# Kernel optimization log

Measured on AMD Instinct MI355X. Metric: run time of the kernel, lower is better.

The kernel has to match this reference:

```python
import math
import jax, jax.numpy as jnp
import numpy as np

DIM = 2048
SLOTS = 256
T = 64          # num_replay_steps
N = 8192        # number of episodic traces
REPLAY_NOISE = 0.01
FREQ = 6.0      # theta frequency (Hz)
DT = 0.01
STRENGTH = 0.5  # write strength used in consolidate()
THRESHOLD = 0.0


def setup_inputs() -> dict:
    key = jax.random.key(0)
    ks = jax.random.split(key, 16)
    def w(k, shape):
        return (jax.random.normal(k, shape, jnp.float32) / math.sqrt(shape[-1]))
    return {
        "traces": jax.random.normal(ks[0], (N, DIM), jnp.float32),
        "noise": jax.random.normal(ks[1], (T, DIM), jnp.float32),
        "memory0": jax.random.normal(ks[2], (SLOTS, DIM), jnp.float32) * 0.01,
        "usage0": jnp.zeros((SLOTS,), jnp.float32),
        "W1": w(ks[3], (DIM, DIM)), "b1": jnp.zeros((DIM,), jnp.float32),
        "W2": w(ks[4], (DIM, DIM)), "b2": jnp.zeros((DIM,), jnp.float32),
        "Wl": w(ks[5], (DIM, DIM)), "bl": jnp.zeros((DIM,), jnp.float32),
        "vw": jax.random.normal(ks[6], (DIM,), jnp.float32),
        "vb": jnp.zeros((DIM,), jnp.float32),
        "Wg": w(ks[7], (DIM, DIM)), "bg": jnp.zeros((DIM,), jnp.float32),
        "Wa": w(ks[8], (SLOTS, DIM)), "ba": jnp.zeros((SLOTS,), jnp.float32),
        "We": w(ks[9], (DIM, DIM)), "be": jnp.zeros((DIM,), jnp.float32),
        "Wad": w(ks[10], (DIM, DIM)), "bad": jnp.zeros((DIM,), jnp.float32),
        "idx": jax.random.randint(ks[11], (T,), 0, N, jnp.int64 if jax.config.jax_enable_x64 else jnp.int32),
    }


def reference(traces, noise, memory0, usage0, W1, b1, W2, b2, Wl, bl, vw, vb,
              Wg, bg, Wa, ba, We, be, Wad, bad, idx):
    # Deterministic theta phase schedule (step_theta per replay step).
    t = jnp.arange(T, dtype=jnp.float32)
    phase = jnp.mod(2.0 * math.pi * FREQ * DT * (t + 1.0), 2.0 * math.pi)  # (T,)

    # --- batched (parallel) part: replay transform + NMDA gate + heads ---
    trace = traces[idx]                                   # (T, DIM) gather
    noisy = trace + noise * REPLAY_NOISE
    h = jax.nn.relu(noisy @ W1.T + b1)
    x = h @ W2.T + b2                                     # transformed (T, DIM)

    ligand = jax.nn.sigmoid(x @ Wl.T + bl)                # (T, DIM)
    phase_signal = jnp.cos(phase - math.pi)[:, None]      # (T, 1)
    voltage = jax.nn.sigmoid(phase_signal * vw[None, :] + vb - THRESHOLD)
    gate = jax.nn.sigmoid((ligand * voltage) @ Wg.T + bg)
    gated = x * gate                                      # (T, DIM)

    logits0 = gated @ Wa.T + ba                           # (T, SLOTS)
    erase = jax.nn.sigmoid(gated @ We.T + be)             # (T, DIM)
    add = gated @ Wad.T + bad                             # (T, DIM)

    # --- sequential part: erase/add outer-product writes with usage penalty ---
    def step(carry, inputs):
        mem, usage = carry
        lg, er, ad = inputs
        wgt = jax.nn.softmax(lg - usage * 0.1)            # (SLOTS,)
        outer_w = STRENGTH * wgt[:, None]                 # (SLOTS, 1)
        mem = mem * (1.0 - outer_w * er[None, :]) + outer_w * ad[None, :]
        return (mem, usage + wgt), None

    (mem, usage), _ = jax.lax.scan(step, (memory0, usage0), (logits0, erase, add))
    return mem
```

## Files before the change

kernel.cpp:

```cpp
#include <hip/hip_runtime.h>
#include <math.h>

#define DIM 2048
#define SLOTS 256
#define TSTEPS 64
#define FB (TSTEPS * DIM)
#define KQ 8
#define KS (DIM / KQ)
#define BK 64
#define NC (KS / BK)
#define JG 32

typedef unsigned short u16;
typedef __bf16 bf16x8 __attribute__((ext_vector_type(8)));
typedef float f32x4 __attribute__((ext_vector_type(4)));

union FragU { unsigned u[4]; bf16x8 v; };

__device__ __forceinline__ u16 f2bf(float f){
    union { float f; unsigned u; } v; v.f = f;
    unsigned r = v.u + 0x7fffu + ((v.u >> 16) & 1u);
    return (u16)(r >> 16);
}
__device__ __forceinline__ float sigmoidf_(float x){ return 1.0f / (1.0f + __expf(-x)); }

__device__ __forceinline__ void split8t(const float* x, bf16x8& hi, bf16x8& lo){
    FragU H, L;
    #pragma unroll
    for (int p = 0; p < 4; ++p){
        union { float f; unsigned u; } u0, u1, l0, l1;
        u0.f = x[2*p]; u1.f = x[2*p+1];
        unsigned h0 = u0.u & 0xffff0000u, h1 = u1.u & 0xffff0000u;
        H.u[p] = (h0 >> 16) | h1;
        l0.f = u0.f - __uint_as_float(h0);
        l1.f = u1.f - __uint_as_float(h1);
        L.u[p] = (l0.u >> 16) | (l1.u & 0xffff0000u);
    }
    hi = H.v; lo = L.v;
}

__device__ __forceinline__ f32x4 mfma16(bf16x8 a, bf16x8 b, f32x4 c){
    return __builtin_amdgcn_mfma_f32_16x16x32_bf16(a, b, c, 0, 0, 0);
}

__device__ __forceinline__ void gl_lds16(const float* gp, float* lp){
    __builtin_amdgcn_global_load_lds(
        (const __attribute__((address_space(1))) unsigned int*)gp,
        (__attribute__((address_space(3))) unsigned int*)lp, 16, 0, 0);
}

__device__ __forceinline__ void calib_inline(int lane, int w, int* trr, int* jrr){
    const u16 oneb = 0x3F80;
    const u16 lb = f2bf((float)((lane & 15) + 1));
    FragU O, L;
    #pragma unroll
    for (int p = 0; p < 4; ++p){
        O.u[p] = ((unsigned)oneb) | (((unsigned)oneb) << 16);
        L.u[p] = ((unsigned)lb)   | (((unsigned)lb)   << 16);
    }
    f32x4 z = {0.f, 0.f, 0.f, 0.f};
    f32x4 dj = mfma16(O.v, L.v, z);
    f32x4 dt = mfma16(L.v, O.v, z);
    #pragma unroll
    for (int r = 0; r < 4; ++r){
        int jl = (int)(dj[r] * (1.0f/32.0f) + 0.5f) - 1;
        int tl = (int)(dt[r] * (1.0f/32.0f) + 0.5f) - 1;
        trr[r] = w * 16 + (tl & 15);
        jrr[r] = jl & 15;
    }
}

struct GSm { float A[NC * 64 * BK]; float Wb[2][16 * BK]; };

__device__ __forceinline__ void gemm_block(const float* __restrict__ A,
                                           const float* __restrict__ Wg0,
                                           int kq, GSm& sm, f32x4* acc)
{
    const int tid = threadIdx.x;
    const int lane = tid & 63, w = tid >> 6;
    const int s = lane & 15, rsub = lane >> 4;
    const int n4 = lane & 15;
    const int kbase = kq * KS;

    #pragma unroll
    for (int c = 0; c < NC; ++c)
        #pragma unroll
        for (int i = 0; i < 4; ++i){
            const int rowL = w * 16 + i * 4 + rsub;
            const float* gp = A + (size_t)rowL * DIM + kbase + c * BK + ((s ^ (rowL & 15)) << 2);
            gl_lds16(gp, sm.A + (c * 64 + w * 16 + i * 4) * BK);
        }
    {
        const int rowL = w * 4 + rsub;
        const float* gp = Wg0 + (size_t)rowL * DIM + kbase + ((s ^ (rowL & 15)) << 2);
        gl_lds16(gp, sm.Wb[0] + (w * 4) * BK);
    }
    __syncthreads();

    acc[0] = (f32x4){0.f, 0.f, 0.f, 0.f};
    acc[1] = (f32x4){0.f, 0.f, 0.f, 0.f};

    #pragma unroll
    for (int it = 0; it < 2 * NC; ++it){
        const int jt = it >> 2, c = it & 3;
        const int bufc = it & 1;
        if (it + 1 < 2 * NC){
            const int nj = (it + 1) >> 2, ncc = (it + 1) & 3;
            const int rowL = w * 4 + rsub;
            const float* gp = Wg0 + (size_t)(nj * 16 + rowL) * DIM
                            + kbase + ncc * BK + ((s ^ (rowL & 15)) << 2);
            gl_lds16(gp, sm.Wb[bufc ^ 1] + (w * 4) * BK);
        }
        const float* At = sm.A + c * 64 * BK;
        const float* Wt = sm.Wb[bufc];
        #pragma unroll
        for (int ks = 0; ks < 2; ++ks){
            const int cg0 = ks * 8 + (lane >> 4) * 2;
            const int rA = w * 16 + n4;
            float a8[8], w8[8];
            *(float4*)(a8)     = *(const float4*)&At[rA * BK + ((cg0 ^ n4) << 2)];
            *(float4*)(a8 + 4) = *(const float4*)&At[rA * BK + (((cg0 + 1) ^ n4) << 2)];
            *(float4*)(w8)     = *(const float4*)&Wt[n4 * BK + ((cg0 ^ n4) << 2)];
            *(float4*)(w8 + 4) = *(const float4*)&Wt[n4 * BK + (((cg0 + 1) ^ n4) << 2)];
            bf16x8 ah, al, wh, wl;
            split8t(a8, ah, al);
            split8t(w8, wh, wl);
            if (jt == 0){
                acc[0] = mfma16(ah, wh, acc[0]);
                acc[0] = mfma16(al, wh, acc[0]);
                acc[0] = mfma16(ah, wl, acc[0]);
            } else {
                acc[1] = mfma16(ah, wh, acc[1]);
                acc[1] = mfma16(al, wh, acc[1]);
                acc[1] = mfma16(ah, wl, acc[1]);
            }
        }
        __syncthreads();
    }
}

__global__ __launch_bounds__(256)
void gemm_s(const float* __restrict__ A, const float* __restrict__ W,
            float* __restrict__ Pp)
{
    __shared__ GSm sm;
    const int kq = blockIdx.x & (KQ - 1);
    const int jg = blockIdx.x >> 3;
    const int j0 = jg * JG;
    const int lane = threadIdx.x & 63, w = threadIdx.x >> 6;
    int trr[4], jrr[4];
    calib_inline(lane, w, trr, jrr);
    f32x4 acc[2];
    gemm_block(A, W + (size_t)j0 * DIM, kq, sm, acc);
    float* outb = Pp + (size_t)kq * FB;
    #pragma unroll
    for (int jt = 0; jt < 2; ++jt)
        #pragma unroll
        for (int r = 0; r < 4; ++r)
            outb[(size_t)trr[r] * DIM + j0 + jt * 16 + jrr[r]] = acc[jt][r];
}

__global__ __launch_bounds__(256)
void gemm_h(const float* __restrict__ G,
            const float* __restrict__ We, const float* __restrict__ Wad,
            const float* __restrict__ Wa,
            float* __restrict__ PpE, float* __restrict__ PpA, float* __restrict__ PpL)
{
    __shared__ GSm sm;
    const int kq = blockIdx.x & (KQ - 1);
    const int jg = blockIdx.x >> 3;
    const float* W; float* out; int j0, NJ;
    if (jg < 64)       { W = We;  out = PpE; j0 = jg * JG;        NJ = DIM; }
    else if (jg < 128) { W = Wad; out = PpA; j0 = (jg - 64) * JG; NJ = DIM; }
    else               { W = Wa;  out = PpL; j0 = (jg - 128) * JG; NJ = SLOTS; }
    const int lane = threadIdx.x & 63, w = threadIdx.x >> 6;
    int trr[4], jrr[4];
    calib_inline(lane, w, trr, jrr);
    f32x4 acc[2];
    gemm_block(G, W + (size_t)j0 * DIM, kq, sm, acc);
    float* outb = out + (size_t)kq * 64 * NJ;
    #pragma unroll
    for (int jt = 0; jt < 2; ++jt)
        #pragma unroll
        for (int r = 0; r < 4; ++r)
            outb[(size_t)trr[r] * NJ + j0 + jt * 16 + jrr[r]] = acc[jt][r];
}

template<int MODE>
__device__ __forceinline__ void comb_core(int bb, const float* __restrict__ P,
    const float* __restrict__ bias, const float* __restrict__ vwp,
    const float* __restrict__ vbp, const float* __restrict__ Xp,
    float* __restrict__ out)
{
    const size_t i0 = ((size_t)bb * 256 + threadIdx.x) * 8;
    const int t = (int)(i0 >> 11);
    const int j = (int)(i0 & (DIM - 1));
    float v[8], tmp[8];
    *(float4*)(v)     = *(const float4*)(P + i0);
    *(float4*)(v + 4) = *(const float4*)(P + i0 + 4);
    #pragma unroll
    for (int p = 1; p < KQ; ++p){
        *(float4*)(tmp)     = *(const float4*)(P + (size_t)p * FB + i0);
        *(float4*)(tmp + 4) = *(const float4*)(P + (size_t)p * FB + i0 + 4);
        #pragma unroll
        for (int c = 0; c < 8; ++c) v[c] += tmp[c];
    }
    float b8[8];
    *(float4*)(b8)     = *(const float4*)(bias + j);
    *(float4*)(b8 + 4) = *(const float4*)(bias + j + 4);
    float x8[8], y8[8];
    if (MODE == 2){
        *(float4*)(x8)     = *(const float4*)(vwp + j);
        *(float4*)(x8 + 4) = *(const float4*)(vwp + j + 4);
        *(float4*)(y8)     = *(const float4*)(vbp + j);
        *(float4*)(y8 + 4) = *(const float4*)(vbp + j + 4);
    }
    if (MODE == 3){
        *(float4*)(x8)     = *(const float4*)(Xp + i0);
        *(float4*)(x8 + 4) = *(const float4*)(Xp + i0 + 4);
    }
    const float ps = -cosf(0.37699111843077515f * (float)(t + 1));
    float r[8];
    #pragma unroll
    for (int c = 0; c < 8; ++c){
        float u = v[c] + b8[c];
        if (MODE == 0)      r[c] = fmaxf(u, 0.f);
        else if (MODE == 1) r[c] = u;
        else if (MODE == 2) r[c] = sigmoidf_(u) * sigmoidf_(fmaf(ps, x8[c], y8[c]));
        else if (MODE == 3) r[c] = x8[c] * sigmoidf_(u);
        else                r[c] = sigmoidf_(u);
    }
    *(float4*)(out + i0)     = *(const float4*)(r);
    *(float4*)(out + i0 + 4) = *(const float4*)(r + 4);
}

template<int MODE>
__global__ __launch_bounds__(256)
void comb8(const float* __restrict__ P, const float* __restrict__ bias,
           const float* __restrict__ vwp, const float* __restrict__ vbp,
           const float* __restrict__ Xp, float* __restrict__ out)
{
    comb_core<MODE>((int)blockIdx.x, P, bias, vwp, vbp, Xp, out);
}

__global__ __launch_bounds__(256)
void comb_ea_scan(const float* __restrict__ PpE, const float* __restrict__ be,
                  const float* __restrict__ PpA, const float* __restrict__ bad_,
                  const float* __restrict__ PpL, const float* __restrict__ ba,
                  const float* __restrict__ usage0,
                  float* __restrict__ ER, float* __restrict__ AD,
                  float* __restrict__ WG)
{
    const int b = (int)blockIdx.x;
    if (b < 64){
        comb_core<4>(b, PpE, be, nullptr, nullptr, nullptr, ER);
        return;
    }
    if (b < 128){
        comb_core<1>(b - 64, PpA, bad_, nullptr, nullptr, nullptr, AD);
        return;
    }
    const int tid = threadIdx.x;
    if (tid >= 64) return;
    const int PS = TSTEPS * SLOTS;
    float u[4], bv[4], cur[4];
    #pragma unroll
    for (int c = 0; c < 4; ++c){
        const int sl = tid + 64 * c;
        u[c]  = usage0[sl];
        bv[c] = ba[sl];
        float s = bv[c];
        #pragma unroll
        for (int p = 0; p < KQ; ++p) s += PpL[p * PS + sl];
        cur[c] = s;
    }
    for (int t = 0; t < TSTEPS; ++t){
        float nxt[4] = {0.f, 0.f, 0.f, 0.f};
        if (t < TSTEPS - 1){
            #pragma unroll
            for (int c = 0; c < 4; ++c){
                const int sl = (t + 1) * SLOTS + tid + 64 * c;
                float s = bv[c];
                #pragma unroll
                for (int p = 0; p < KQ; ++p) s += PpL[p * PS + sl];
                nxt[c] = s;
            }
        }
        float e[4];
        #pragma unroll
        for (int c = 0; c < 4; ++c) e[c] = __expf(cur[c] - 0.1f * u[c]);
        float sm_ = (e[0] + e[1]) + (e[2] + e[3]);
        #pragma unroll
        for (int off = 1; off < 64; off <<= 1) sm_ += __shfl_xor(sm_, off, 64);
        float inv = 1.0f / sm_;
        float* wr = WG + t * SLOTS;
        #pragma unroll
        for (int c = 0; c < 4; ++c){
            float ww = e[c] * inv;
            u[c] += ww;
            wr[tid + 64 * c] = ww;
        }
        #pragma unroll
        for (int c = 0; c < 4; ++c) cur[c] = nxt[c];
    }
}

__global__ __launch_bounds__(256)
void init_k(const float* __restrict__ traces, const float* __restrict__ noise,
            const int* __restrict__ idxw, float* __restrict__ A0)
{
    const int tid = threadIdx.x;
    __shared__ int i64f;
    int v = 0;
    if (tid < 32) v = (idxw[2 * tid + 1] != 0) ? 1 : 0;
    unsigned long long bm = __ballot(v);
    if (tid == 0) i64f = (bm == 0ull) ? 1 : 0;
    __syncthreads();
    const int t = blockIdx.x;
    long row = i64f ? (long)idxw[2 * t] : (long)idxw[t];
    const int k = tid * 8;
    const float* tr = traces + (size_t)row * DIM + k;
    const float* nz = noise + (size_t)t * DIM + k;
    float4 a0 = *(const float4*)(tr), a1 = *(const float4*)(tr + 4);
    float4 b0 = *(const float4*)(nz), b1 = *(const float4*)(nz + 4);
    float4 r0, r1;
    r0.x = fmaf(0.01f, b0.x, a0.x); r0.y = fmaf(0.01f, b0.y, a0.y);
    r0.z = fmaf(0.01f, b0.z, a0.z); r0.w = fmaf(0.01f, b0.w, a0.w);
    r1.x = fmaf(0.01f, b1.x, a1.x); r1.y = fmaf(0.01f, b1.y, a1.y);
    r1.z = fmaf(0.01f, b1.z, a1.z); r1.w = fmaf(0.01f, b1.w, a1.w);
    float* o = A0 + (size_t)t * DIM + k;
    *(float4*)(o) = r0; *(float4*)(o + 4) = r1;
}

__global__ __launch_bounds__(256)
void mem_k(const float* __restrict__ mem0, const float* __restrict__ wgt,
           const float* __restrict__ ER, const float* __restrict__ AD,
           float* __restrict__ out)
{
    const int s = threadIdx.x;
    const int d0 = blockIdx.x * 8;
    float m[8];
    *(float4*)(m)     = *(const float4*)(mem0 + (size_t)s * DIM + d0);
    *(float4*)(m + 4) = *(const float4*)(mem0 + (size_t)s * DIM + d0 + 4);
    for (int t = 0; t < TSTEPS; ++t){
        const size_t ro = (size_t)t * DIM + d0;
        float e8[8], a8[8];
        *(float4*)(e8)     = *(const float4*)(ER + ro);
        *(float4*)(e8 + 4) = *(const float4*)(ER + ro + 4);
        *(float4*)(a8)     = *(const float4*)(AD + ro);
        *(float4*)(a8 + 4) = *(const float4*)(AD + ro + 4);
        float w = 0.5f * wgt[t * SLOTS + s];
        #pragma unroll
        for (int c = 0; c < 8; ++c){
            float f = w * e8[c];
            float tmp = fmaf(-f, m[c], m[c]);
            m[c] = fmaf(w, a8[c], tmp);
        }
    }
    float* op = out + (size_t)s * DIM + d0;
    *(float4*)(op)     = *(const float4*)(m);
    *(float4*)(op + 4) = *(const float4*)(m + 4);
}

extern "C" void kernel_launch(void* const* d_in, const int* in_sizes, int n_in,
                              void* d_out, int out_size, void* d_ws, size_t ws_size,
                              hipStream_t stream)
{
    const float* traces = (const float*)d_in[0];
    const float* noise  = (const float*)d_in[1];
    const float* mem0   = (const float*)d_in[2];
    const float* usage0 = (const float*)d_in[3];
    const float* W1 = (const float*)d_in[4];  const float* b1 = (const float*)d_in[5];
    const float* W2 = (const float*)d_in[6];  const float* b2 = (const float*)d_in[7];
    const float* Wl = (const float*)d_in[8];  const float* bl = (const float*)d_in[9];
    const float* vw = (const float*)d_in[10]; const float* vb = (const float*)d_in[11];
    const float* Wg = (const float*)d_in[12]; const float* bg = (const float*)d_in[13];
    const float* Wa = (const float*)d_in[14]; const float* ba = (const float*)d_in[15];
    const float* We = (const float*)d_in[16]; const float* be = (const float*)d_in[17];
    const float* Wad = (const float*)d_in[18]; const float* bad_ = (const float*)d_in[19];
    const int* idx = (const int*)d_in[20];

    float* pool = (float*)d_ws;
    float* A0v = pool + 0 * (size_t)FB;
    float* Hv  = pool + 1 * (size_t)FB;
    float* Xv  = pool + 2 * (size_t)FB;
    float* LVv = pool + 3 * (size_t)FB;
    float* Gv  = pool + 4 * (size_t)FB;
    float* ERv = pool + 5 * (size_t)FB;
    float* ADv = pool + 6 * (size_t)FB;
    float* Pp  = pool + 7 * (size_t)FB;
    float* PpE = pool + 15 * (size_t)FB;
    float* PpA = pool + 23 * (size_t)FB;
    float* PpL = pool + 31 * (size_t)FB;
    float* WGv = pool + 32 * (size_t)FB;

    init_k<<<TSTEPS, 256, 0, stream>>>(traces, noise, idx, A0v);

    gemm_s<<<64 * KQ, 256, 0, stream>>>(A0v, W1, Pp);
    comb8<0><<<64, 256, 0, stream>>>(Pp, b1, nullptr, nullptr, nullptr, Hv);
    gemm_s<<<64 * KQ, 256, 0, stream>>>(Hv, W2, Pp);
    comb8<1><<<64, 256, 0, stream>>>(Pp, b2, nullptr, nullptr, nullptr, Xv);
    gemm_s<<<64 * KQ, 256, 0, stream>>>(Xv, Wl, Pp);
    comb8<2><<<64, 256, 0, stream>>>(Pp, bl, vw, vb, nullptr, LVv);
    gemm_s<<<64 * KQ, 256, 0, stream>>>(LVv, Wg, Pp);
    comb8<3><<<64, 256, 0, stream>>>(Pp, bg, nullptr, nullptr, Xv, Gv);

    gemm_h<<<136 * KQ, 256, 0, stream>>>(Gv, We, Wad, Wa, PpE, PpA, PpL);
    comb_ea_scan<<<129, 256, 0, stream>>>(PpE, be, PpA, bad_, PpL, ba, usage0,
                                          ERv, ADv, WGv);
    mem_k<<<DIM / 8, 256, 0, stream>>>(mem0, WGv, ERv, ADv, (float*)d_out);
}
```

Baseline: 290.1 us.

## Fuse gather into first GEMM and fuse scan, combine and memory update

The gather-plus-noise step is folded into the first GEMM's A-tile load, so the init kernel and its round trip through global memory go away. The softmax scan, the erase/add split-K reduction and the memory update are merged into one kernel. Each of its 256 blocks recomputes the softmax weights into shared memory and reduces the partial sums on the fly. W-tile staging switches from async global-to-LDS loads to register prefetch two chunks ahead, with explicit barriers. The cost is redundant scan work in every block and more global reads of the partial sums per block, in exchange for two fewer launches and fewer intermediate buffers.

Measured after the change: 416.8 us. 1.44x slower.

```diff
diff --git a/kernel.cpp b/kernel.cpp
--- a/kernel.cpp
+++ b/kernel.cpp
@@ -72,9 +72,18 @@
 
 struct GSm { float A[NC * 64 * BK]; float Wb[2][16 * BK]; };
 
-__device__ __forceinline__ void gemm_block(const float* __restrict__ A,
-                                           const float* __restrict__ Wg0,
-                                           int kq, GSm& sm, f32x4* acc)
+__device__ __forceinline__ const float* waddr(const float* Wg0, int kbase, int chunk,
+                                              int w, int rsub, int s){
+    const int rowL = w * 4 + rsub;
+    const int nj = chunk >> 2, ncc = chunk & 3;
+    return Wg0 + (size_t)(nj * 16 + rowL) * DIM + kbase + ncc * BK + ((s ^ rowL) << 2);
+}
+
+template<int GATHER>
+__device__ __forceinline__ void gemm_core(const float* __restrict__ A,
+    const float* __restrict__ traces, const float* __restrict__ noise,
+    const int* __restrict__ idxw, int i64f,
+    const float* __restrict__ Wg0, int kq, GSm& sm, f32x4* acc)
 {
     const int tid = threadIdx.x;
     const int lane = tid & 63, w = tid >> 6;
@@ -82,19 +91,35 @@
     const int n4 = lane & 15;
     const int kbase = kq * KS;
 
-    #pragma unroll
-    for (int c = 0; c < NC; ++c)
+    if (GATHER){
         #pragma unroll
         for (int i = 0; i < 4; ++i){
             const int rowL = w * 16 + i * 4 + rsub;
-            const float* gp = A + (size_t)rowL * DIM + kbase + c * BK + ((s ^ (rowL & 15)) << 2);
-            gl_lds16(gp, sm.A + (c * 64 + w * 16 + i * 4) * BK);
-        }
-    {
-        const int rowL = w * 4 + rsub;
-        const float* gp = Wg0 + (size_t)rowL * DIM + kbase + ((s ^ (rowL & 15)) << 2);
-        gl_lds16(gp, sm.Wb[0] + (w * 4) * BK);
-    }
+            long rg = i64f ? (long)idxw[2 * rowL] : (long)idxw[rowL];
+            const float* tp = traces + (size_t)rg * DIM + kbase + ((s ^ (rowL & 15)) << 2);
+            const float* np = noise + (size_t)rowL * DIM + kbase + ((s ^ (rowL & 15)) << 2);
+            #pragma unroll
+            for (int c = 0; c < NC; ++c){
+                float4 tv = *(const float4*)(tp + c * BK);
+                float4 nv = *(const float4*)(np + c * BK);
+                float4 r;
+                r.x = fmaf(0.01f, nv.x, tv.x); r.y = fmaf(0.01f, nv.y, tv.y);
+                r.z = fmaf(0.01f, nv.z, tv.z); r.w = fmaf(0.01f, nv.w, tv.w);
+                *(float4*)&sm.A[(c * 64 + rowL) * BK + s * 4] = r;
+            }
+        }
+    } else {
+        #pragma unroll
+        for (int c = 0; c < NC; ++c)
+            #pragma unroll
+            for (int i = 0; i < 4; ++i){
+                const int rowL = w * 16 + i * 4 + rsub;
+                const float* gp = A + (size_t)rowL * DIM + kbase + c * BK + ((s ^ (rowL & 15)) << 2);
+                gl_lds16(gp, sm.A + (c * 64 + w * 16 + i * 4) * BK);
+            }
+    }
+    float4 wr0 = *(const float4*)waddr(Wg0, kbase, 0, w, rsub, s);
+    float4 wr1 = *(const float4*)waddr(Wg0, kbase, 1, w, rsub, s);
     __syncthreads();
 
     acc[0] = (f32x4){0.f, 0.f, 0.f, 0.f};
@@ -102,17 +127,20 @@
 
     #pragma unroll
     for (int it = 0; it < 2 * NC; ++it){
+        const int slot = it & 1;
+        if (slot == 0){
+            *(float4*)&sm.Wb[0][(w * 4 + rsub) * BK + s * 4] = wr0;
+            if (it + 2 < 2 * NC)
+                wr0 = *(const float4*)waddr(Wg0, kbase, it + 2, w, rsub, s);
+        } else {
+            *(float4*)&sm.Wb[1][(w * 4 + rsub) * BK + s * 4] = wr1;
+            if (it + 2 < 2 * NC)
+                wr1 = *(const float4*)waddr(Wg0, kbase, it + 2, w, rsub, s);
+        }
+        asm volatile("s_waitcnt lgkmcnt(0)\n\ts_barrier" ::: "memory");
         const int jt = it >> 2, c = it & 3;
-        const int bufc = it & 1;
-        if (it + 1 < 2 * NC){
-            const int nj = (it + 1) >> 2, ncc = (it + 1) & 3;
-            const int rowL = w * 4 + rsub;
-            const float* gp = Wg0 + (size_t)(nj * 16 + rowL) * DIM
-                            + kbase + ncc * BK + ((s ^ (rowL & 15)) << 2);
-            gl_lds16(gp, sm.Wb[bufc ^ 1] + (w * 4) * BK);
-        }
         const float* At = sm.A + c * 64 * BK;
-        const float* Wt = sm.Wb[bufc];
+        const float* Wt = sm.Wb[slot];
         #pragma unroll
         for (int ks = 0; ks < 2; ++ks){
             const int cg0 = ks * 8 + (lane >> 4) * 2;
@@ -135,8 +163,39 @@
                 acc[1] = mfma16(ah, wl, acc[1]);
             }
         }
-        __syncthreads();
-    }
+        asm volatile("s_barrier" ::: "memory");
+    }
+}
+
+__global__ __launch_bounds__(256)
+void gemm_g1(const float* __restrict__ traces, const float* __restrict__ noise,
+             const int* __restrict__ idxw, const float* __restrict__ W,
+             float* __restrict__ Pp)
+{
+    __shared__ GSm sm;
+    __shared__ int i64f_s;
+    const int tid = threadIdx.x;
+    int v = 0;
+    if (tid < 32) v = (idxw[2 * tid + 1] != 0) ? 1 : 0;
+    unsigned long long bm = __ballot(v);
+    if (tid == 0) i64f_s = (bm == 0ull) ? 1 : 0;
+    __syncthreads();
+    const int i64f = i64f_s;
+
+    const int kq = blockIdx.x & (KQ - 1);
+    const int jg = blockIdx.x >> 3;
+    const int j0 = jg * JG;
+    const int lane = tid & 63, w = tid >> 6;
+    int trr[4], jrr[4];
+    calib_inline(lane, w, trr, jrr);
+    f32x4 acc[2];
+    gemm_core<1>(nullptr, traces, noise, idxw, i64f, W + (size_t)j0 * DIM, kq, sm, acc);
+    float* outb = Pp + (size_t)kq * FB;
+    #pragma unroll
+    for (int jt = 0; jt < 2; ++jt)
+        #pragma unroll
+        for (int r = 0; r < 4; ++r)
+            outb[(size_t)trr[r] * DIM + j0 + jt * 16 + jrr[r]] = acc[jt][r];
 }
 
 __global__ __launch_bounds__(256)
@@ -151,7 +210,7 @@
     int trr[4], jrr[4];
     calib_inline(lane, w, trr, jrr);
     f32x4 acc[2];
-    gemm_block(A, W + (size_t)j0 * DIM, kq, sm, acc);
+    gemm_core<0>(A, nullptr, nullptr, nullptr, 0, W + (size_t)j0 * DIM, kq, sm, acc);
     float* outb = Pp + (size_t)kq * FB;
     #pragma unroll
     for (int jt = 0; jt < 2; ++jt)
@@ -177,7 +236,7 @@
     int trr[4], jrr[4];
     calib_inline(lane, w, trr, jrr);
     f32x4 acc[2];
-    gemm_block(G, W + (size_t)j0 * DIM, kq, sm, acc);
+    gemm_core<0>(G, nullptr, nullptr, nullptr, 0, W + (size_t)j0 * DIM, kq, sm, acc);
     float* outb = out + (size_t)kq * 64 * NJ;
     #pragma unroll
     for (int jt = 0; jt < 2; ++jt)
@@ -187,12 +246,12 @@
 }
 
 template<int MODE>
-__device__ __forceinline__ void comb_core(int bb, const float* __restrict__ P,
-    const float* __restrict__ bias, const float* __restrict__ vwp,
-    const float* __restrict__ vbp, const float* __restrict__ Xp,
-    float* __restrict__ out)
-{
-    const size_t i0 = ((size_t)bb * 256 + threadIdx.x) * 8;
+__global__ __launch_bounds__(256)
+void comb8(const float* __restrict__ P, const float* __restrict__ bias,
+           const float* __restrict__ vwp, const float* __restrict__ vbp,
+           const float* __restrict__ Xp, float* __restrict__ out)
+{
+    const size_t i0 = ((size_t)blockIdx.x * 256 + threadIdx.x) * 8;
     const int t = (int)(i0 >> 11);
     const int j = (int)(i0 & (DIM - 1));
     float v[8], tmp[8];
@@ -227,134 +286,102 @@
         if (MODE == 0)      r[c] = fmaxf(u, 0.f);
         else if (MODE == 1) r[c] = u;
         else if (MODE == 2) r[c] = sigmoidf_(u) * sigmoidf_(fmaf(ps, x8[c], y8[c]));
-        else if (MODE == 3) r[c] = x8[c] * sigmoidf_(u);
-        else                r[c] = sigmoidf_(u);
+        else                r[c] = x8[c] * sigmoidf_(u);
     }
     *(float4*)(out + i0)     = *(const float4*)(r);
     *(float4*)(out + i0 + 4) = *(const float4*)(r + 4);
 }
 
-template<int MODE>
 __global__ __launch_bounds__(256)
-void comb8(const float* __restrict__ P, const float* __restrict__ bias,
-           const float* __restrict__ vwp, const float* __restrict__ vbp,
-           const float* __restrict__ Xp, float* __restrict__ out)
-{
-    comb_core<MODE>((int)blockIdx.x, P, bias, vwp, vbp, Xp, out);
-}
-
-__global__ __launch_bounds__(256)
-void comb_ea_scan(const float* __restrict__ PpE, const float* __restrict__ be,
-                  const float* __restrict__ PpA, const float* __restrict__ bad_,
-                  const float* __restrict__ PpL, const float* __restrict__ ba,
-                  const float* __restrict__ usage0,
-                  float* __restrict__ ER, float* __restrict__ AD,
-                  float* __restrict__ WG)
-{
-    const int b = (int)blockIdx.x;
-    if (b < 64){
-        comb_core<4>(b, PpE, be, nullptr, nullptr, nullptr, ER);
-        return;
-    }
-    if (b < 128){
-        comb_core<1>(b - 64, PpA, bad_, nullptr, nullptr, nullptr, AD);
-        return;
-    }
+void memscan_k(const float* __restrict__ PpL, const float* __restrict__ ba,
+               const float* __restrict__ usage0,
+               const float* __restrict__ PpE, const float* __restrict__ be,
+               const float* __restrict__ PpA, const float* __restrict__ bad_,
+               const float* __restrict__ mem0, float* __restrict__ out)
+{
+    __shared__ float wg[TSTEPS][SLOTS];
     const int tid = threadIdx.x;
-    if (tid >= 64) return;
-    const int PS = TSTEPS * SLOTS;
-    float u[4], bv[4], cur[4];
-    #pragma unroll
-    for (int c = 0; c < 4; ++c){
-        const int sl = tid + 64 * c;
-        u[c]  = usage0[sl];
-        bv[c] = ba[sl];
-        float s = bv[c];
-        #pragma unroll
-        for (int p = 0; p < KQ; ++p) s += PpL[p * PS + sl];
-        cur[c] = s;
-    }
-    for (int t = 0; t < TSTEPS; ++t){
-        float nxt[4] = {0.f, 0.f, 0.f, 0.f};
-        if (t < TSTEPS - 1){
+
+    if (tid < 64){
+        const int PS = TSTEPS * SLOTS;
+        float u[4], bv[4], cur[4];
+        #pragma unroll
+        for (int c = 0; c < 4; ++c){
+            const int sl = tid + 64 * c;
+            u[c]  = usage0[sl];
+            bv[c] = ba[sl];
+            float sv = bv[c];
+            #pragma unroll
+            for (int p = 0; p < KQ; ++p) sv += PpL[p * PS + sl];
+            cur[c] = sv;
+        }
+        for (int t = 0; t < TSTEPS; ++t){
+            float nxt[4] = {0.f, 0.f, 0.f, 0.f};
+            if (t < TSTEPS - 1){
+                #pragma unroll
+                for (int c = 0; c < 4; ++c){
+                    const int sl = (t + 1) * SLOTS + tid + 64 * c;
+                    float sv = bv[c];
+                    #pragma unroll
+                    for (int p = 0; p < KQ; ++p) sv += PpL[p * PS + sl];
+                    nxt[c] = sv;
+                }
+            }
+            float e[4];
+            #pragma unroll
+            for (int c = 0; c < 4; ++c) e[c] = __expf(cur[c] - 0.1f * u[c]);
+            float sm_ = (e[0] + e[1]) + (e[2] + e[3]);
+            #pragma unroll
+            for (int off = 1; off < 64; off <<= 1) sm_ += __shfl_xor(sm_, off, 64);
+            float inv = 1.0f / sm_;
             #pragma unroll
             for (int c = 0; c < 4; ++c){
-                const int sl = (t + 1) * SLOTS + tid + 64 * c;
-                float s = bv[c];
-                #pragma unroll
-                for (int p = 0; p < KQ; ++p) s += PpL[p * PS + sl];
-                nxt[c] = s;
+                float ww = e[c] * inv;
+                u[c] += ww;
+                wg[t][tid + 64 * c] = ww;
             }
-        }
-        float e[4];
-        #pragma unroll
-        for (int c = 0; c < 4; ++c) e[c] = __expf(cur[c] - 0.1f * u[c]);
-        float sm_ = (e[0] + e[1]) + (e[2] + e[3]);
-        #pragma unroll
-        for (int off = 1; off < 64; off <<= 1) sm_ += __shfl_xor(sm_, off, 64);
-        float inv = 1.0f / sm_;
-        float* wr = WG + t * SLOTS;
-        #pragma unroll
-        for (int c = 0; c < 4; ++c){
-            float ww = e[c] * inv;
-            u[c] += ww;
-            wr[tid + 64 * c] = ww;
-        }
-        #pragma unroll
-        for (int c = 0; c < 4; ++c) cur[c] = nxt[c];
-    }
-}
-
-__global__ __launch_bounds__(256)
-void init_k(const float* __restrict__ traces, const float* __restrict__ noise,
-            const int* __restrict__ idxw, float* __restrict__ A0)
-{
-    const int tid = threadIdx.x;
-    __shared__ int i64f;
-    int v = 0;
-    if (tid < 32) v = (idxw[2 * tid + 1] != 0) ? 1 : 0;
-    unsigned long long bm = __ballot(v);
-    if (tid == 0) i64f = (bm == 0ull) ? 1 : 0;
+            #pragma unroll
+            for (int c = 0; c < 4; ++c) cur[c] = nxt[c];
+        }
+    }
     __syncthreads();
-    const int t = blockIdx.x;
-    long row = i64f ? (long)idxw[2 * t] : (long)idxw[t];
-    const int k = tid * 8;
-    const float* tr = traces + (size_t)row * DIM + k;
-    const float* nz = noise + (size_t)t * DIM + k;
-    float4 a0 = *(const float4*)(tr), a1 = *(const float4*)(tr + 4);
-    float4 b0 = *(const float4*)(nz), b1 = *(const float4*)(nz + 4);
-    float4 r0, r1;
-    r0.x = fmaf(0.01f, b0.x, a0.x); r0.y = fmaf(0.01f, b0.y, a0.y);
-    r0.z = fmaf(0.01f, b0.z, a0.z); r0.w = fmaf(0.01f, b0.w, a0.w);
-    r1.x = fmaf(0.01f, b1.x, a1.x); r1.y = fmaf(0.01f, b1.y, a1.y);
-    r1.z = fmaf(0.01f, b1.z, a1.z); r1.w = fmaf(0.01f, b1.w, a1.w);
-    float* o = A0 + (size_t)t * DIM + k;
-    *(float4*)(o) = r0; *(float4*)(o + 4) = r1;
-}
-
-__global__ __launch_bounds__(256)
-void mem_k(const float* __restrict__ mem0, const float* __restrict__ wgt,
-           const float* __restrict__ ER, const float* __restrict__ AD,
-           float* __restrict__ out)
-{
-    const int s = threadIdx.x;
-    const int d0 = blockIdx.x * 8;
+
+    const int s = tid;
+    const int d0 = (int)blockIdx.x * 8;
+    float b_e[8], b_a[8];
+    *(float4*)(b_e)     = *(const float4*)(be + d0);
+    *(float4*)(b_e + 4) = *(const float4*)(be + d0 + 4);
+    *(float4*)(b_a)     = *(const float4*)(bad_ + d0);
+    *(float4*)(b_a + 4) = *(const float4*)(bad_ + d0 + 4);
     float m[8];
     *(float4*)(m)     = *(const float4*)(mem0 + (size_t)s * DIM + d0);
     *(float4*)(m + 4) = *(const float4*)(mem0 + (size_t)s * DIM + d0 + 4);
     for (int t = 0; t < TSTEPS; ++t){
         const size_t ro = (size_t)t * DIM + d0;
-        float e8[8], a8[8];
-        *(float4*)(e8)     = *(const float4*)(ER + ro);
-        *(float4*)(e8 + 4) = *(const float4*)(ER + ro + 4);
-        *(float4*)(a8)     = *(const float4*)(AD + ro);
-        *(float4*)(a8 + 4) = *(const float4*)(AD + ro + 4);
-        float w = 0.5f * wgt[t * SLOTS + s];
+        float e8[8], a8[8], tmp[8];
+        *(float4*)(e8)     = *(const float4*)(PpE + ro);
+        *(float4*)(e8 + 4) = *(const float4*)(PpE + ro + 4);
+        *(float4*)(a8)     = *(const float4*)(PpA + ro);
+        *(float4*)(a8 + 4) = *(const float4*)(PpA + ro + 4);
+        #pragma unroll
+        for (int p = 1; p < KQ; ++p){
+            *(float4*)(tmp)     = *(const float4*)(PpE + (size_t)p * FB + ro);
+            *(float4*)(tmp + 4) = *(const float4*)(PpE + (size_t)p * FB + ro + 4);
+            #pragma unroll
+            for (int c = 0; c < 8; ++c) e8[c] += tmp[c];
+            *(float4*)(tmp)     = *(const float4*)(PpA + (size_t)p * FB + ro);
+            *(float4*)(tmp + 4) = *(const float4*)(PpA + (size_t)p * FB + ro + 4);
+            #pragma unroll
+            for (int c = 0; c < 8; ++c) a8[c] += tmp[c];
+        }
+        float wq = 0.5f * wg[t][s];
         #pragma unroll
         for (int c = 0; c < 8; ++c){
-            float f = w * e8[c];
-            float tmp = fmaf(-f, m[c], m[c]);
-            m[c] = fmaf(w, a8[c], tmp);
+            float er = sigmoidf_(e8[c] + b_e[c]);
+            float ad = a8[c] + b_a[c];
+            float f = wq * er;
+            float tmp2 = fmaf(-f, m[c], m[c]);
+            m[c] = fmaf(wq, ad, tmp2);
         }
     }
     float* op = out + (size_t)s * DIM + d0;
@@ -381,22 +408,16 @@
     const int* idx = (const int*)d_in[20];
 
     float* pool = (float*)d_ws;
-    float* A0v = pool + 0 * (size_t)FB;
-    float* Hv  = pool + 1 * (size_t)FB;
-    float* Xv  = pool + 2 * (size_t)FB;
-    float* LVv = pool + 3 * (size_t)FB;
-    float* Gv  = pool + 4 * (size_t)FB;
-    float* ERv = pool + 5 * (size_t)FB;
-    float* ADv = pool + 6 * (size_t)FB;
-    float* Pp  = pool + 7 * (size_t)FB;
-    float* PpE = pool + 15 * (size_t)FB;
-    float* PpA = pool + 23 * (size_t)FB;
-    float* PpL = pool + 31 * (size_t)FB;
-    float* WGv = pool + 32 * (size_t)FB;
-
-    init_k<<<TSTEPS, 256, 0, stream>>>(traces, noise, idx, A0v);
-
-    gemm_s<<<64 * KQ, 256, 0, stream>>>(A0v, W1, Pp);
+    float* Hv  = pool + 0 * (size_t)FB;
+    float* Xv  = pool + 1 * (size_t)FB;
+    float* LVv = pool + 2 * (size_t)FB;
+    float* Gv  = pool + 3 * (size_t)FB;
+    float* Pp  = pool + 4 * (size_t)FB;
+    float* PpE = pool + 12 * (size_t)FB;
+    float* PpA = pool + 20 * (size_t)FB;
+    float* PpL = pool + 28 * (size_t)FB;
+
+    gemm_g1<<<64 * KQ, 256, 0, stream>>>(traces, noise, idx, W1, Pp);
     comb8<0><<<64, 256, 0, stream>>>(Pp, b1, nullptr, nullptr, nullptr, Hv);
     gemm_s<<<64 * KQ, 256, 0, stream>>>(Hv, W2, Pp);
     comb8<1><<<64, 256, 0, stream>>>(Pp, b2, nullptr, nullptr, nullptr, Xv);
@@ -406,7 +427,6 @@
     comb8<3><<<64, 256, 0, stream>>>(Pp, bg, nullptr, nullptr, Xv, Gv);
 
     gemm_h<<<136 * KQ, 256, 0, stream>>>(Gv, We, Wad, Wa, PpE, PpA, PpL);
-    comb_ea_scan<<<129, 256, 0, stream>>>(PpE, be, PpA, bad_, PpL, ba, usage0,
-                                          ERv, ADv, WGv);
-    mem_k<<<DIM / 8, 256, 0, stream>>>(mem0, WGv, ERv, ADv, (float*)d_out);
-}
+    memscan_k<<<DIM / 8, 256, 0, stream>>>(PpL, ba, usage0, PpE, be, PpA, bad_,
+                                           mem0, (float*)d_out);
+}
```
